# Kernel optimization log

Measured on AMD Instinct MI355X. Metric: run time of the kernel, lower is better.

## Reference

```python
import jax, jax.numpy as jnp
import numpy as np

DIM = 256
HEADS = 8
HEAD_DIM = DIM // HEADS
HIDDEN = DIM * 4


def layer_norm(x, w, b, eps=1e-5):
    m = jnp.mean(x, axis=-1, keepdims=True)
    v = jnp.mean((x - m) ** 2, axis=-1, keepdims=True)
    return (x - m) / jnp.sqrt(v + eps) * w + b


def setup_inputs() -> dict:
    key = jax.random.key(0)
    ks = jax.random.split(key, 12)
    s = lambda fan_in: 1.0 / np.sqrt(fan_in)
    inp = {
        "x0": jax.random.normal(ks[0], (2, 32, 64, DIM), jnp.float32),
        "x1": jax.random.normal(ks[1], (2, 32, 64, DIM), jnp.float32),
        # torch Linear weights stored [out, in], no bias for qk/v/merge
        "qk_w": jax.random.uniform(ks[2], (DIM, DIM), jnp.float32, -s(DIM), s(DIM)),
        "v_w": jax.random.uniform(ks[3], (DIM, DIM), jnp.float32, -s(DIM), s(DIM)),
        "merge_w": jax.random.uniform(ks[4], (DIM, DIM), jnp.float32, -s(DIM), s(DIM)),
        "ln1_w": jnp.ones((DIM,), jnp.float32),
        "ln1_b": jnp.zeros((DIM,), jnp.float32),
        "ln2_w": jnp.ones((DIM,), jnp.float32),
        "ln2_b": jnp.zeros((DIM,), jnp.float32),
        "fc1_w": jax.random.uniform(ks[5], (HIDDEN, 2 * DIM), jnp.float32, -s(2 * DIM), s(2 * DIM)),
        "fc1_b": jnp.zeros((HIDDEN,), jnp.float32),
        "fc2_w": jax.random.uniform(ks[6], (DIM, HIDDEN), jnp.float32, -s(HIDDEN), s(HIDDEN)),
        "fc2_b": jnp.zeros((DIM,), jnp.float32),
        "gamma": jnp.ones((DIM,), jnp.float32),
    }
    return inp


def reference(x0, x1, qk_w, v_w, merge_w, ln1_w, ln1_b, ln2_w, ln2_b,
              fc1_w, fc1_b, fc2_w, fc2_b, gamma):
    N0, L0, WW0, C = x0.shape
    N1, L1, WW1, _ = x1.shape
    x0f = x0.reshape(N0, L0 * WW0, C)
    x1f = x1.reshape(N1, L1 * WW1, C)

    n0 = layer_norm(x0f, ln1_w, ln1_b)
    n1 = layer_norm(x1f, ln1_w, ln1_b)

    def heads(t):  # [N, S, C] -> [N, H, S, Dh]
        N, S, _ = t.shape
        return t.reshape(N, S, HEADS, HEAD_DIM).transpose(0, 2, 1, 3)

    scale = HEAD_DIM ** -0.25  # sqrt of softmax_temp, applied to both sides
    qk0 = heads(n0 @ qk_w.T) * scale
    qk1 = heads(n1 @ qk_w.T) * scale
    v0 = heads(n0 @ v_w.T)
    v1 = heads(n1 @ v_w.T)

    # shared score matrix, reused for both softmax directions
    sim = jnp.einsum('bhld,bhsd->bhls', qk0, qk1)  # [N,H,L,S]
    attn01 = jax.nn.softmax(sim, axis=-1)
    attn10 = jax.nn.softmax(sim, axis=-2)  # == softmax(sim^T, -1)^T

    m0 = jnp.einsum('bhls,bhsd->bhld', attn01, v1)
    m1 = jnp.einsum('bhls,bhld->bhsd', attn10, v0)

    def unheads(t):  # [N,H,S,Dh] -> [N,S,C]
        N, H, S, D = t.shape
        return t.transpose(0, 2, 1, 3).reshape(N, S, H * D)

    m0 = unheads(m0) @ merge_w.T
    m1 = unheads(m1) @ merge_w.T

    def ffn_residual(x, m):
        h = jnp.concatenate([x, m], axis=-1)
        h = jax.nn.gelu(h @ fc1_w.T + fc1_b, approximate=False)
        h = h @ fc2_w.T + fc2_b
        return x + gamma * layer_norm(h, ln2_w, ln2_b)

    y0 = ffn_residual(x0f, m0).reshape(N0, L0, WW0, C)
    y1 = ffn_residual(x1f, m1).reshape(N1, L1, WW1, C)
    return (y0, y1)
```

## Files before the change

### kernel.cpp

```cpp
#include <hip/hip_runtime.h>
#include <hip/hip_bf16.h>
#include <math.h>


typedef float  f32x4  __attribute__((ext_vector_type(4)));
typedef __bf16 bf16x8 __attribute__((ext_vector_type(8)));

#define MFMA16(A, B, C) __builtin_amdgcn_mfma_f32_16x16x32_bf16((A), (B), (C), 0, 0, 0)

static constexpr int   ROWS  = 8192;
static constexpr float QK_SCALE = 0.42044820762685725f * 1.2011224087864498f;

__device__ inline unsigned short f2b(float f) {
    __hip_bfloat16 h = __float2bfloat16(f);
    union { __hip_bfloat16 h; unsigned short u; } cv;
    cv.h = h;
    return cv.u;
}

__device__ inline float exp2_fast(float x) {
#if __has_builtin(__builtin_amdgcn_exp2f)
    return __builtin_amdgcn_exp2f(x);
#else
    return __exp2f(x);
#endif
}

__device__ inline float gelu_f(float x) {
    float z = 0.7978845608028654f * (x + 0.044715f * x * x * x);
    z = fminf(fmaxf(z, -15.0f), 15.0f);
    const float e = __expf(-2.0f * z);
    const float t = (1.0f - e) / (1.0f + e);
    return 0.5f * x * (1.0f + t);
}

__global__ __launch_bounds__(256) void prep_kernel(
    const float* __restrict__ qkw, const float* __restrict__ vw,
    const float* __restrict__ mw,  const float* __restrict__ w1,
    const float* __restrict__ w2,  unsigned short* __restrict__ o,
    const float* __restrict__ x0,  const float* __restrict__ x1,
    const float* __restrict__ lw,  const float* __restrict__ lb,
    unsigned short* __restrict__ nb, unsigned short* __restrict__ acat)
{
    __shared__ unsigned short As[64 * 72];
    __shared__ unsigned short Ws[64 * 72];
    if (blockIdx.x < 2560) {
        int i = blockIdx.x * 256 + threadIdx.x;
        if      (i <  65536) o[i] = f2b(qkw[i]);
        else if (i < 131072) o[i] = f2b(vw[i - 65536]);
        else if (i < 393216) {
            int j = i - 131072, r = j >> 8, c = j & 255;
            o[131072 + r * 512 + c] = f2b(w1[(size_t)r * 512 + c]);
        } else {
            o[i + 262144] = f2b(w2[i - 393216]);
        }
        return;
    }
    if (blockIdx.x < 4608) {
        const int wid  = threadIdx.x >> 6;
        const int lane = threadIdx.x & 63;
        const int row  = (blockIdx.x - 2560) * 4 + wid;
        const float* xr = (row < 4096) ? (x0 + (size_t)row * 256)
                                       : (x1 + (size_t)(row - 4096) * 256);
        const int c0 = lane * 4;
        const float4 xv = *(const float4*)(xr + c0);
        float s  = (xv.x + xv.y) + (xv.z + xv.w);
        float sq = (xv.x * xv.x + xv.y * xv.y) + (xv.z * xv.z + xv.w * xv.w);
#pragma unroll
        for (int off = 1; off < 64; off <<= 1) {
            s  += __shfl_xor(s,  off);
            sq += __shfl_xor(sq, off);
        }
        const float mean = s * (1.0f / 256.0f);
        const float var  = sq * (1.0f / 256.0f) - mean * mean;
        const float rs   = rsqrtf(var + 1e-5f);
        const float4 wv4 = *(const float4*)(lw + c0);
        const float4 bv4 = *(const float4*)(lb + c0);
        ushort4 nv;
        nv.x = f2b((xv.x - mean) * rs * wv4.x + bv4.x);
        nv.y = f2b((xv.y - mean) * rs * wv4.y + bv4.y);
        nv.z = f2b((xv.z - mean) * rs * wv4.z + bv4.z);
        nv.w = f2b((xv.w - mean) * rs * wv4.w + bv4.w);
        *(ushort4*)(nb + (size_t)row * 256 + c0) = nv;
        ushort4 xb;
        xb.x = f2b(xv.x); xb.y = f2b(xv.y); xb.z = f2b(xv.z); xb.w = f2b(xv.w);
        *(ushort4*)(acat + (size_t)row * 512 + c0) = xb;
        return;
    }
    const int t   = blockIdx.x - 4608;
    const int i0  = (t >> 2) * 64;
    const int j0  = (t & 3) * 64;
    const int tid  = threadIdx.x;
    const int wid  = tid >> 6;
    const int lane = tid & 63;
    const int ln   = lane & 15;
    const int quad = lane >> 4;
    f32x4 acc[4] = {{0,0,0,0},{0,0,0,0},{0,0,0,0},{0,0,0,0}};
    const int srow = tid >> 3;
    const int skc  = (tid & 7) * 8;
    for (int k0 = 0; k0 < 256; k0 += 64) {
#pragma unroll
        for (int rr = 0; rr < 2; ++rr) {
            const int row = srow + rr * 32;
            const float* asrc = w1 + (size_t)(i0 + row) * 512 + 256 + k0 + skc;
            const float4 f0 = *(const float4*)(asrc);
            const float4 f1 = *(const float4*)(asrc + 4);
            ushort4 a0, a1;
            a0.x = f2b(f0.x); a0.y = f2b(f0.y); a0.z = f2b(f0.z); a0.w = f2b(f0.w);
            a1.x = f2b(f1.x); a1.y = f2b(f1.y); a1.z = f2b(f1.z); a1.w = f2b(f1.w);
            *(ushort4*)(As + row * 72 + skc)     = a0;
            *(ushort4*)(As + row * 72 + skc + 4) = a1;
            const float* bsrc = mw + (size_t)(k0 + skc) * 256 + (j0 + row);
            ushort4 b0, b1;
            b0.x = f2b(bsrc[0 * 256]); b0.y = f2b(bsrc[1 * 256]);
            b0.z = f2b(bsrc[2 * 256]); b0.w = f2b(bsrc[3 * 256]);
            b1.x = f2b(bsrc[4 * 256]); b1.y = f2b(bsrc[5 * 256]);
            b1.z = f2b(bsrc[6 * 256]); b1.w = f2b(bsrc[7 * 256]);
            *(ushort4*)(Ws + row * 72 + skc)     = b0;
            *(ushort4*)(Ws + row * 72 + skc + 4) = b1;
        }
        __syncthreads();
#pragma unroll
        for (int kk = 0; kk < 64; kk += 32) {
            const bf16x8 af = *(const bf16x8*)(As + (wid * 16 + ln) * 72 + kk + quad * 8);
#pragma unroll
            for (int f = 0; f < 4; ++f) {
                const bf16x8 wf = *(const bf16x8*)(Ws + (f * 16 + ln) * 72 + kk + quad * 8);
                acc[f] = MFMA16(wf, af, acc[f]);
            }
        }
        __syncthreads();
    }
    const int rowm = i0 + wid * 16 + ln;
#pragma unroll
    for (int f = 0; f < 4; ++f) {
        const int cb = j0 + f * 16 + quad * 4;
        ushort4 ov;
        ov.x = f2b(acc[f][0]); ov.y = f2b(acc[f][1]);
        ov.z = f2b(acc[f][2]); ov.w = f2b(acc[f][3]);
        *(ushort4*)(o + 131072 + (size_t)rowm * 512 + 256 + cb) = ov;
    }
}

__global__ __launch_bounds__(256) void gemm_qkv(
    const unsigned short* __restrict__ A, const unsigned short* __restrict__ W,
    unsigned short* __restrict__ qkb, unsigned short* __restrict__ vtb)
{
    constexpr int K = 256;
    __shared__ unsigned short As[64 * 72];
    __shared__ unsigned short Ws[64 * 72];
    const int tid  = threadIdx.x;
    const int wid  = tid >> 6;
    const int lane = tid & 63;
    const int ln   = lane & 15;
    const int quad = lane >> 4;
    const int m0 = blockIdx.x * 64, n0 = blockIdx.y * 64;
    f32x4 acc[4] = {{0,0,0,0},{0,0,0,0},{0,0,0,0},{0,0,0,0}};
    const int srow = tid >> 3;
    const int skc  = (tid & 7) * 8;
    const unsigned short* aP0 = A + (size_t)(m0 + srow)      * K + skc;
    const unsigned short* aP1 = A + (size_t)(m0 + srow + 32) * K + skc;
    const unsigned short* wP0 = W + (size_t)(n0 + srow)      * K + skc;
    const unsigned short* wP1 = W + (size_t)(n0 + srow + 32) * K + skc;
    for (int k0 = 0; k0 < K; k0 += 64) {
        *(uint4*)(As + srow * 72 + skc)        = *(const uint4*)(aP0 + k0);
        *(uint4*)(As + (srow + 32) * 72 + skc) = *(const uint4*)(aP1 + k0);
        *(uint4*)(Ws + srow * 72 + skc)        = *(const uint4*)(wP0 + k0);
        *(uint4*)(Ws + (srow + 32) * 72 + skc) = *(const uint4*)(wP1 + k0);
        __syncthreads();
#pragma unroll
        for (int kk = 0; kk < 64; kk += 32) {
            const bf16x8 af = *(const bf16x8*)(As + (wid * 16 + ln) * 72 + kk + quad * 8);
#pragma unroll
            for (int f = 0; f < 4; ++f) {
                const bf16x8 wf = *(const bf16x8*)(Ws + (f * 16 + ln) * 72 + kk + quad * 8);
                acc[f] = MFMA16(wf, af, acc[f]);
            }
        }
        __syncthreads();
    }
    const int rowm = m0 + wid * 16 + ln;
    if (n0 < 256) {
#pragma unroll
        for (int f = 0; f < 4; ++f) {
            const int cb = n0 + f * 16 + quad * 4;
            ushort4 o;
            o.x = f2b(acc[f][0] * QK_SCALE); o.y = f2b(acc[f][1] * QK_SCALE);
            o.z = f2b(acc[f][2] * QK_SCALE); o.w = f2b(acc[f][3] * QK_SCALE);
            *(ushort4*)(qkb + (size_t)rowm * 256 + cb) = o;
        }
    } else {
#pragma unroll
        for (int f = 0; f < 4; ++f) {
            const int cb = (n0 - 256) + f * 16 + quad * 4;
#pragma unroll
            for (int r = 0; r < 4; ++r)
                vtb[(size_t)(cb + r) * 8192 + rowm] = f2b(acc[f][r]);
        }
    }
}

template <bool GELU_, bool OUTB>
__global__ __launch_bounds__(256) void gemm128(
    const unsigned short* __restrict__ A, const unsigned short* __restrict__ W,
    const float* __restrict__ bias,
    unsigned short* __restrict__ outB, float* __restrict__ outF,
    int K, int NS)
{
    __shared__ unsigned short As[128 * 72];
    __shared__ unsigned short Ws[128 * 72];
    const int tid  = threadIdx.x;
    const int wid  = tid >> 6;
    const int lane = tid & 63;
    const int ln   = lane & 15;
    const int quad = lane >> 4;
    const int m0 = blockIdx.x * 128, n0 = blockIdx.y * 128;
    const int wm = (wid & 1) * 64, wn = (wid >> 1) * 64;
    f32x4 acc[4][4];
#pragma unroll
    for (int f = 0; f < 4; ++f)
#pragma unroll
        for (int i = 0; i < 4; ++i) acc[f][i] = (f32x4){0, 0, 0, 0};
    const int sr = tid >> 2;
    const int sc = (tid & 3) * 8;
    for (int k0 = 0; k0 < K; k0 += 64) {
        const unsigned short* aB = A + (size_t)m0 * K + k0;
        const unsigned short* wB = W + (size_t)n0 * K + k0;
        *(uint4*)(As + sr * 72 + sc)             = *(const uint4*)(aB + (size_t)sr * K + sc);
        *(uint4*)(As + sr * 72 + sc + 32)        = *(const uint4*)(aB + (size_t)sr * K + sc + 32);
        *(uint4*)(As + (sr + 64) * 72 + sc)      = *(const uint4*)(aB + (size_t)(sr + 64) * K + sc);
        *(uint4*)(As + (sr + 64) * 72 + sc + 32) = *(const uint4*)(aB + (size_t)(sr + 64) * K + sc + 32);
        *(uint4*)(Ws + sr * 72 + sc)             = *(const uint4*)(wB + (size_t)sr * K + sc);
        *(uint4*)(Ws + sr * 72 + sc + 32)        = *(const uint4*)(wB + (size_t)sr * K + sc + 32);
        *(uint4*)(Ws + (sr + 64) * 72 + sc)      = *(const uint4*)(wB + (size_t)(sr + 64) * K + sc);
        *(uint4*)(Ws + (sr + 64) * 72 + sc + 32) = *(const uint4*)(wB + (size_t)(sr + 64) * K + sc + 32);
        __syncthreads();
#pragma unroll
        for (int kk = 0; kk < 64; kk += 32) {
            bf16x8 af[4], wf[4];
#pragma unroll
            for (int i = 0; i < 4; ++i)
                af[i] = *(const bf16x8*)(As + (wm + i * 16 + ln) * 72 + kk + quad * 8);
#pragma unroll
            for (int f = 0; f < 4; ++f)
                wf[f] = *(const bf16x8*)(Ws + (wn + f * 16 + ln) * 72 + kk + quad * 8);
#pragma unroll
            for (int f = 0; f < 4; ++f)
#pragma unroll
                for (int i = 0; i < 4; ++i)
                    acc[f][i] = MFMA16(wf[f], af[i], acc[f][i]);
        }
        __syncthreads();
    }
#pragma unroll
    for (int f = 0; f < 4; ++f) {
        const int feat = n0 + wn + f * 16 + quad * 4;
        const float4 b4 = *(const float4*)(bias + feat);
#pragma unroll
        for (int i = 0; i < 4; ++i) {
            const int token = m0 + wm + i * 16 + ln;
            float vv[4] = {acc[f][i][0] + b4.x, acc[f][i][1] + b4.y,
                           acc[f][i][2] + b4.z, acc[f][i][3] + b4.w};
            if (GELU_) {
#pragma unroll
                for (int r = 0; r < 4; ++r) vv[r] = gelu_f(vv[r]);
            }
            if (OUTB) {
                ushort4 o;
                o.x = f2b(vv[0]); o.y = f2b(vv[1]); o.z = f2b(vv[2]); o.w = f2b(vv[3]);
                *(ushort4*)(outB + (size_t)token * NS + feat) = o;
            } else {
                float4 o = {vv[0], vv[1], vv[2], vv[3]};
                *(float4*)(outF + (size_t)token * NS + feat) = o;
            }
        }
    }
}

__global__ __launch_bounds__(256, 4) void attn_kernel(
    const unsigned short* __restrict__ qk, const unsigned short* __restrict__ vtb,
    unsigned short* __restrict__ mo)
{
    __shared__ unsigned short Pw[4][64 * 32];
    const int tid  = threadIdx.x;
    const int wid  = tid >> 6;
    const int lane = tid & 63;
    const int ln   = lane & 15;
    const int quad = lane >> 4;
    const int dir = blockIdx.z, bh = blockIdx.y;
    const int b = bh >> 3, h = bh & 7;
    const int qbase = b * 2048 + (dir ? 4096 : 0);
    const int kbase = b * 2048 + (dir ? 0 : 4096);
    const int q0 = blockIdx.x * 64;
    const int xsw = ((ln >> 1) & 1) << 4;

    bf16x8 qf[4];
#pragma unroll
    for (int qg = 0; qg < 4; ++qg)
        qf[qg] = *(const bf16x8*)(qk + (size_t)(qbase + q0 + qg * 16 + ln) * 256 + h * 32 + quad * 8);

    f32x4 oacc[4][2];
#pragma unroll
    for (int qg = 0; qg < 4; ++qg) {
        oacc[qg][0] = (f32x4){0, 0, 0, 0};
        oacc[qg][1] = (f32x4){0, 0, 0, 0};
    }
    float lp[4] = {0.0f, 0.0f, 0.0f, 0.0f};
    const f32x4 zf = {0, 0, 0, 0};

    const unsigned short* kp = qk  + (size_t)(kbase + wid * 32 + ln) * 256 + h * 32 + quad * 8;
    const unsigned short* vp = vtb + (size_t)(h * 32 + ln) * 8192 + (kbase + wid * 32) + quad * 8;

    unsigned short* Pq[4];
#pragma unroll
    for (int qg = 0; qg < 4; ++qg) Pq[qg] = &Pw[wid][(qg * 16 + ln) * 32];

    bf16x8 kc0 = *(const bf16x8*)(kp);
    bf16x8 kc1 = *(const bf16x8*)(kp + 16 * 256);
    bf16x8 vc0 = *(const bf16x8*)(vp);
    bf16x8 vc1 = *(const bf16x8*)(vp + 16 * 8192);
    bf16x8 kn0, kn1, vn0, vn1;

    for (int it = 0; it < 16; ++it) {
#pragma unroll
        for (int sub = 0; sub < 2; ++sub) {
            const bf16x8 kf = sub ? kc1 : kc0;
            f32x4 s[4];
#pragma unroll
            for (int qg = 0; qg < 4; ++qg) s[qg] = MFMA16(kf, qf[qg], zf);
#pragma unroll
            for (int qg = 0; qg < 4; ++qg) {
                const float e0 = exp2_fast(s[qg][0]), e1 = exp2_fast(s[qg][1]);
                const float e2 = exp2_fast(s[qg][2]), e3 = exp2_fast(s[qg][3]);
                lp[qg] += (e0 + e1) + (e2 + e3);
                ushort4 pb;
                pb.x = f2b(e0); pb.y = f2b(e1); pb.z = f2b(e2); pb.w = f2b(e3);
                *(ushort4*)(Pq[qg] + ((sub * 16 + quad * 4) ^ xsw)) = pb;
            }
        }
        if (it < 15) {
            const unsigned short* kpn = kp + (size_t)(it + 1) * 128 * 256;
            const unsigned short* vpn = vp + (it + 1) * 128;
            kn0 = *(const bf16x8*)(kpn);
            kn1 = *(const bf16x8*)(kpn + 16 * 256);
            vn0 = *(const bf16x8*)(vpn);
            vn1 = *(const bf16x8*)(vpn + 16 * 8192);
        }
        asm volatile("s_waitcnt lgkmcnt(0)" ::: "memory");
#pragma unroll
        for (int qg = 0; qg < 4; ++qg) {
            const bf16x8 pf = *(const bf16x8*)(Pq[qg] + ((quad * 8) ^ xsw));
            oacc[qg][0] = MFMA16(vc0, pf, oacc[qg][0]);
            oacc[qg][1] = MFMA16(vc1, pf, oacc[qg][1]);
        }
        if (it < 15) { kc0 = kn0; kc1 = kn1; vc0 = vn0; vc1 = vn1; }
    }

#pragma unroll
    for (int qg = 0; qg < 4; ++qg) {
        lp[qg] += __shfl_xor(lp[qg], 16);
        lp[qg] += __shfl_xor(lp[qg], 32);
    }
    __syncthreads();
    float* scr  = (float*)&Pw[0][0];
    float* Lbuf = scr;
    float* Obuf = scr + 256;
    if (quad == 0) {
#pragma unroll
        for (int qg = 0; qg < 4; ++qg) Lbuf[wid * 64 + qg * 16 + ln] = lp[qg];
    }
#pragma unroll
    for (int qg = 0; qg < 4; ++qg) {
#pragma unroll
        for (int dg = 0; dg < 2; ++dg)
            *(f32x4*)&Obuf[(wid * 2 + dg) * 256 + lane * 4] = oacc[qg][dg];
        __syncthreads();
        if (wid == qg) {
            const int q = qg * 16 + ln;
            const float rinv = 1.0f /
                (Lbuf[q] + Lbuf[64 + q] + Lbuf[128 + q] + Lbuf[192 + q]);
            const size_t orow = (size_t)(qbase + q0 + q) * 512 + 256 + h * 32;
#pragma unroll
            for (int dg = 0; dg < 2; ++dg) {
                f32x4 sum = *(f32x4*)&Obuf[(0 + dg) * 256 + lane * 4];
#pragma unroll
                for (int w = 1; w < 4; ++w)
                    sum += *(f32x4*)&Obuf[(w * 2 + dg) * 256 + lane * 4];
                ushort4 o;
                o.x = f2b(sum[0] * rinv); o.y = f2b(sum[1] * rinv);
                o.z = f2b(sum[2] * rinv); o.w = f2b(sum[3] * rinv);
                *(ushort4*)(mo + orow + dg * 16 + quad * 4) = o;
            }
        }
        __syncthreads();
    }
}

__global__ __launch_bounds__(256) void ln_out_kernel(
    const float* __restrict__ x0, const float* __restrict__ x1,
    const float* __restrict__ h2, const float* __restrict__ w,
    const float* __restrict__ b,  const float* __restrict__ gamma,
    float* __restrict__ out)
{
    const int wid  = threadIdx.x >> 6;
    const int lane = threadIdx.x & 63;
    const int row  = blockIdx.x * 4 + wid;
    const int c0 = lane * 4;
    const float4 hv = *(const float4*)(h2 + (size_t)row * 256 + c0);
    float s  = (hv.x + hv.y) + (hv.z + hv.w);
    float sq = (hv.x * hv.x + hv.y * hv.y) + (hv.z * hv.z + hv.w * hv.w);
#pragma unroll
    for (int off = 1; off < 64; off <<= 1) {
        s  += __shfl_xor(s,  off);
        sq += __shfl_xor(sq, off);
    }
    const float mean = s * (1.0f / 256.0f);
    const float var  = sq * (1.0f / 256.0f) - mean * mean;
    const float rs   = rsqrtf(var + 1e-5f);
    const float* xr = (row < 4096) ? (x0 + (size_t)row * 256)
                                   : (x1 + (size_t)(row - 4096) * 256);
    const float4 xv = *(const float4*)(xr + c0);
    const float4 w4 = *(const float4*)(w + c0);
    const float4 b4 = *(const float4*)(b + c0);
    const float4 g4 = *(const float4*)(gamma + c0);
    float4 y;
    y.x = xv.x + g4.x * ((hv.x - mean) * rs * w4.x + b4.x);
    y.y = xv.y + g4.y * ((hv.y - mean) * rs * w4.y + b4.y);
    y.z = xv.z + g4.z * ((hv.z - mean) * rs * w4.z + b4.z);
    y.w = xv.w + g4.w * ((hv.w - mean) * rs * w4.w + b4.w);
    *(float4*)(out + (size_t)row * 256 + c0) = y;
}

extern "C" void kernel_launch(void* const* d_in, const int* in_sizes, int n_in,
                              void* d_out, int out_size, void* d_ws, size_t ws_size,
                              hipStream_t stream) {
    (void)in_sizes; (void)n_in; (void)out_size; (void)ws_size;
    const float* x0      = (const float*)d_in[0];
    const float* x1      = (const float*)d_in[1];
    const float* qk_w    = (const float*)d_in[2];
    const float* v_w     = (const float*)d_in[3];
    const float* merge_w = (const float*)d_in[4];
    const float* ln1_w   = (const float*)d_in[5];
    const float* ln1_b   = (const float*)d_in[6];
    const float* ln2_w   = (const float*)d_in[7];
    const float* ln2_b   = (const float*)d_in[8];
    const float* fc1_w   = (const float*)d_in[9];
    const float* fc1_b   = (const float*)d_in[10];
    const float* fc2_w   = (const float*)d_in[11];
    const float* fc2_b   = (const float*)d_in[12];
    const float* gamma   = (const float*)d_in[13];
    float* out = (float*)d_out;

    unsigned short* nb   = (unsigned short*)d_ws;
    unsigned short* qkb  = nb   + (size_t)ROWS * 256;
    unsigned short* vtb  = qkb  + (size_t)ROWS * 256;
    unsigned short* acat = vtb  + (size_t)ROWS * 256;
    unsigned short* fc1o = acat + (size_t)ROWS * 512;
    float*          h2   = (float*)(fc1o + (size_t)ROWS * 1024);
    unsigned short* wqv  = (unsigned short*)(h2 + (size_t)ROWS * 256);
    unsigned short* w1f  = wqv + 131072;
    unsigned short* w2b  = w1f + 524288;

    prep_kernel<<<4672, 256, 0, stream>>>(
        qk_w, v_w, merge_w, fc1_w, fc2_w, wqv,
        x0, x1, ln1_w, ln1_b, nb, acat);

    gemm_qkv<<<dim3(128, 8), 256, 0, stream>>>(nb, wqv, qkb, vtb);

    attn_kernel<<<dim3(32, 16, 2), 256, 0, stream>>>(qkb, vtb, acat);

    gemm128<true, true><<<dim3(64, 8), 256, 0, stream>>>(
        acat, w1f, fc1_b, fc1o, nullptr, 512, 1024);
    gemm128<false, false><<<dim3(64, 2), 256, 0, stream>>>(
        fc1o, w2b, fc2_b, nullptr, h2, 1024, 256);

    ln_out_kernel<<<2048, 256, 0, stream>>>(x0, x1, h2, ln2_w, ln2_b, gamma, out);
}
```

Before: 183.7 us.

## Split attention key range across two blocks and reduce partials in new kernel

The attention kernel now splits each direction's 2048-key range into two halves on separate blocks, doubling the grid from 1024 to 2048 blocks. Each block writes unnormalized fp32 partial outputs and row sums to workspace. A new reduce kernel combines the two halves, normalizes, and writes bf16 into the concat buffer. This adds parallelism on a chip with many CUs, at the cost of an extra launch and about 16 MB of fp32 partial traffic.

Result: slower. 190.5 us (+3.7%).

```diff
diff --git a/kernel.cpp b/kernel.cpp
--- a/kernel.cpp
+++ b/kernel.cpp
@@ -279,7 +279,7 @@
 
 __global__ __launch_bounds__(256, 4) void attn_kernel(
     const unsigned short* __restrict__ qk, const unsigned short* __restrict__ vtb,
-    unsigned short* __restrict__ mo)
+    float* __restrict__ pO, float* __restrict__ pL)
 {
     __shared__ unsigned short Pw[4][64 * 32];
     const int tid  = threadIdx.x;
@@ -287,10 +287,11 @@
     const int lane = tid & 63;
     const int ln   = lane & 15;
     const int quad = lane >> 4;
-    const int dir = blockIdx.z, bh = blockIdx.y;
+    const int half = blockIdx.z & 1, dir = blockIdx.z >> 1;
+    const int bh = blockIdx.y;
     const int b = bh >> 3, h = bh & 7;
     const int qbase = b * 2048 + (dir ? 4096 : 0);
-    const int kbase = b * 2048 + (dir ? 0 : 4096);
+    const int kbase = b * 2048 + (dir ? 0 : 4096) + half * 1024;
     const int q0 = blockIdx.x * 64;
     const int xsw = ((ln >> 1) & 1) << 4;
 
@@ -321,7 +322,7 @@
     bf16x8 vc1 = *(const bf16x8*)(vp + 16 * 8192);
     bf16x8 kn0, kn1, vn0, vn1;
 
-    for (int it = 0; it < 16; ++it) {
+    for (int it = 0; it < 8; ++it) {
 #pragma unroll
         for (int sub = 0; sub < 2; ++sub) {
             const bf16x8 kf = sub ? kc1 : kc0;
@@ -338,7 +339,7 @@
                 *(ushort4*)(Pq[qg] + ((sub * 16 + quad * 4) ^ xsw)) = pb;
             }
         }
-        if (it < 15) {
+        if (it < 7) {
             const unsigned short* kpn = kp + (size_t)(it + 1) * 128 * 256;
             const unsigned short* vpn = vp + (it + 1) * 128;
             kn0 = *(const bf16x8*)(kpn);
@@ -353,7 +354,7 @@
             oacc[qg][0] = MFMA16(vc0, pf, oacc[qg][0]);
             oacc[qg][1] = MFMA16(vc1, pf, oacc[qg][1]);
         }
-        if (it < 15) { kc0 = kn0; kc1 = kn1; vc0 = vn0; vc1 = vn1; }
+        if (it < 7) { kc0 = kn0; kc1 = kn1; vc0 = vn0; vc1 = vn1; }
     }
 
 #pragma unroll
@@ -377,23 +378,39 @@
         __syncthreads();
         if (wid == qg) {
             const int q = qg * 16 + ln;
-            const float rinv = 1.0f /
-                (Lbuf[q] + Lbuf[64 + q] + Lbuf[128 + q] + Lbuf[192 + q]);
-            const size_t orow = (size_t)(qbase + q0 + q) * 512 + 256 + h * 32;
+            const int row = qbase + q0 + q;
+            if (quad == 0)
+                pL[(size_t)half * ROWS * 8 + (size_t)row * 8 + h] =
+                    Lbuf[q] + Lbuf[64 + q] + Lbuf[128 + q] + Lbuf[192 + q];
 #pragma unroll
             for (int dg = 0; dg < 2; ++dg) {
                 f32x4 sum = *(f32x4*)&Obuf[(0 + dg) * 256 + lane * 4];
 #pragma unroll
                 for (int w = 1; w < 4; ++w)
                     sum += *(f32x4*)&Obuf[(w * 2 + dg) * 256 + lane * 4];
-                ushort4 o;
-                o.x = f2b(sum[0] * rinv); o.y = f2b(sum[1] * rinv);
-                o.z = f2b(sum[2] * rinv); o.w = f2b(sum[3] * rinv);
-                *(ushort4*)(mo + orow + dg * 16 + quad * 4) = o;
-            }
-        }
-        __syncthreads();
-    }
+                *(f32x4*)(pO + ((size_t)half * ROWS + row) * 256
+                             + h * 32 + dg * 16 + quad * 4) = sum;
+            }
+        }
+        __syncthreads();
+    }
+}
+
+__global__ __launch_bounds__(256) void attn_reduce(
+    const float* __restrict__ pO, const float* __restrict__ pL,
+    unsigned short* __restrict__ acat)
+{
+    const int row = blockIdx.x * 4 + (threadIdx.x >> 6);
+    const int c0  = (threadIdx.x & 63) * 4;
+    const int h   = c0 >> 5;
+    const f32x4 o0 = *(const f32x4*)(pO + (size_t)row * 256 + c0);
+    const f32x4 o1 = *(const f32x4*)(pO + ((size_t)ROWS + row) * 256 + c0);
+    const float L  = pL[(size_t)row * 8 + h] + pL[(size_t)ROWS * 8 + (size_t)row * 8 + h];
+    const float rinv = 1.0f / L;
+    ushort4 o;
+    o.x = f2b((o0[0] + o1[0]) * rinv); o.y = f2b((o0[1] + o1[1]) * rinv);
+    o.z = f2b((o0[2] + o1[2]) * rinv); o.w = f2b((o0[3] + o1[3]) * rinv);
+    *(ushort4*)(acat + (size_t)row * 512 + 256 + c0) = o;
 }
 
 __global__ __launch_bounds__(256) void ln_out_kernel(
@@ -460,6 +477,8 @@
     unsigned short* wqv  = (unsigned short*)(h2 + (size_t)ROWS * 256);
     unsigned short* w1f  = wqv + 131072;
     unsigned short* w2b  = w1f + 524288;
+    float*          pO   = (float*)(w2b + 262144);
+    float*          pL   = pO + (size_t)2 * ROWS * 256;
 
     prep_kernel<<<4672, 256, 0, stream>>>(
         qk_w, v_w, merge_w, fc1_w, fc2_w, wqv,
@@ -467,7 +486,8 @@
 
     gemm_qkv<<<dim3(128, 8), 256, 0, stream>>>(nb, wqv, qkb, vtb);
 
-    attn_kernel<<<dim3(32, 16, 2), 256, 0, stream>>>(qkb, vtb, acat);
+    attn_kernel<<<dim3(32, 16, 4), 256, 0, stream>>>(qkb, vtb, pO, pL);
+    attn_reduce<<<2048, 256, 0, stream>>>(pO, pL, acat);
 
     gemm128<true, true><<<dim3(64, 8), 256, 0, stream>>>(
         acat, w1f, fc1_b, fc1o, nullptr, 512, 1024);
```
